# Performance work log

Hardware: AMD Instinct MI355X
Metric: run time of the kernel (lower is better)

The kernel has to match this reference:

```python
import jax, jax.numpy as jnp
import numpy as np

B, L, N_KERNELS = 16, 4096, 512
KSS = [7, 9, 11]


def _make_params():
    """Replicates ROCKET.__init__ random kernel generation (numpy RNG, seed 0).

    Note: the torch code builds Conv1d with padding=2*padding (padding doubled),
    computes the padding from the *float* dilation, and casts dilation to int
    for the conv. We reproduce that exactly.
    """
    rng = np.random.default_rng(0)
    ks_a, d_a, pad_a, w_l, b_l = [], [], [], [], []
    for _ in range(N_KERNELS):
        ks = int(rng.choice(KSS))
        d_f = 2.0 ** rng.uniform(0.0, np.log2((L - 1) // (ks - 1)))
        d = int(d_f)
        p0 = int((ks - 1) * d_f // 2) if rng.integers(2) == 1 else 0
        pad = 2 * p0  # conv1d padding arg is 2*padding in the source
        w = rng.standard_normal(ks).astype(np.float32)
        w -= w.mean()  # weight -= weight.mean() (c_in=1 -> mean over ks)
        b = np.float32(2.0 * (rng.random() - 0.5))
        ks_a.append(ks); d_a.append(d); pad_a.append(pad)
        w_l.append(w); b_l.append(b)
    P = max(pad_a)  # global pad applied once to x; per-kernel offset corrects
    groups = {}
    order = []
    for ks in KSS:
        ids = [i for i in range(N_KERNELS) if ks_a[i] == ks]
        order += ids
        off = np.stack([[P - pad_a[i] + k * d_a[i] for k in range(ks)] for i in ids]).astype(np.int32)
        lout = np.array([L + 2 * pad_a[i] - d_a[i] * (ks - 1) for i in ids], np.int32)
        w = np.stack([w_l[i] for i in ids]).astype(np.float32)
        b = np.array([b_l[i] for i in ids], np.float32)
        groups[ks] = (w, b, off, lout)
    perm = np.argsort(np.array(order)).astype(np.int32)  # grouped -> original order
    return groups, perm, P


def setup_inputs() -> dict:
    key = jax.random.key(0)
    x = jax.random.normal(key, (B, 1, L), dtype=jnp.float32)
    groups, perm, P = _make_params()
    inp = {"x": x, "perm": jnp.asarray(perm), "P": int(P)}
    for gi, ks in enumerate(KSS):
        w, b, off, lout = groups[ks]
        inp[f"w{gi}"] = jnp.asarray(w)
        inp[f"b{gi}"] = jnp.asarray(b)
        inp[f"off{gi}"] = jnp.asarray(off)
        inp[f"lout{gi}"] = jnp.asarray(lout)
    return inp


def _group_feats(x_pad, w, b, off, lout, Lmax, Lp):
    # x_pad: [B, Lp]; w: [G, ks]; off: [G, ks]; lout: [G]
    t = jnp.arange(Lmax)
    out = b[None, :, None]  # [1, G, 1]
    ks = w.shape[-1]
    for k in range(ks):  # ks <= 11 taps of the dilated conv, batched over G kernels
        idx = jnp.clip(off[:, k][:, None] + t[None, :], 0, Lp - 1)  # [G, Lmax]
        out = out + w[:, k][None, :, None] * x_pad[:, idx]  # [B, G, Lmax]
    valid = (t[None, :] < lout[:, None])[None]  # [1, G, Lmax]
    mx = jnp.max(jnp.where(valid, out, jnp.finfo(out.dtype).min), axis=-1)  # [B, G]
    ppv = jnp.where(valid, out > 0, False).sum(-1).astype(out.dtype) / lout[None, :].astype(out.dtype)
    return mx, ppv


def reference(x, w0, b0, off0, lout0, w1, b1, off1, lout1, w2, b2, off2, lout2, perm, P):
    xs = x[:, 0, :]  # c_in = 1
    Lseq = xs.shape[-1]
    Lmax = 2 * Lseq + 16  # static bound: lout <= 2L + max(ks)
    Lp = Lseq + 2 * P
    x_pad = jnp.pad(xs, ((0, 0), (P, P)))
    mxs, ppvs = [], []
    for (w, b, off, lout) in ((w0, b0, off0, lout0), (w1, b1, off1, lout1), (w2, b2, off2, lout2)):
        mx, ppv = _group_feats(x_pad, w, b, off, lout, Lmax, Lp)
        mxs.append(mx)
        ppvs.append(ppv)
    mx = jnp.concatenate(mxs, axis=1)[:, perm]   # [B, n_kernels] original order
    ppv = jnp.concatenate(ppvs, axis=1)[:, perm]
    # torch.cat interleaves (max_i, ppv_i) along feature dim
    return jnp.stack([mx, ppv], axis=2).reshape(x.shape[0], -1)
```

## Files before the change

### kernel.cpp

```cpp
#include <hip/hip_runtime.h>
#include <math.h>

#define LSEQ 4096
#define NK 512
#define NB 16

template <int KS>
__device__ __forceinline__ void rocket_body(
    const float* __restrict__ sx,
    const float* __restrict__ w, const float* __restrict__ bias,
    const int* __restrict__ off, const int* __restrict__ lout,
    int P, int li, int b, int outj,
    float* __restrict__ out, float* smx, int* scnt)
{
    const int tid = threadIdx.x;

    float wk[KS];
#pragma unroll
    for (int k = 0; k < KS; ++k) wk[k] = w[li * KS + k];
    const int o0  = off[li * KS + 0];
    const int o1  = off[li * KS + 1];
    const int d   = o1 - o0;
    const int pad = P - o0;
    const float bi = bias[li];
    const int   Lo = lout[li];

    int t_lo = min(pad, Lo);
    int t_hi = min(Lo, LSEQ - (KS - 1) * d + pad);
    if (t_hi < t_lo) t_hi = t_lo;

    float mx  = -INFINITY;
    int   cnt = 0;

    for (int t = tid; t < t_lo; t += 256) {
        float y = bi;
        int idx = t - pad;
#pragma unroll
        for (int k = 0; k < KS; ++k) {
            int ic = min(max(idx, 0), LSEQ - 1);
            float xv = sx[ic];
            xv = ((unsigned)idx < (unsigned)LSEQ) ? xv : 0.0f;
            y = fmaf(wk[k], xv, y);
            idx += d;
        }
        mx = fmaxf(mx, y); cnt += (y > 0.0f);
    }

    for (int t = t_lo + tid; t < t_hi; t += 256) {
        const float* p = sx + (t - pad);
        float y = bi;
#pragma unroll
        for (int k = 0; k < KS; ++k) y = fmaf(wk[k], p[k * d], y);
        mx = fmaxf(mx, y); cnt += (y > 0.0f);
    }

    for (int t = t_hi + tid; t < Lo; t += 256) {
        float y = bi;
        int idx = t - pad;
#pragma unroll
        for (int k = 0; k < KS; ++k) {
            int ic = min(max(idx, 0), LSEQ - 1);
            float xv = sx[ic];
            xv = ((unsigned)idx < (unsigned)LSEQ) ? xv : 0.0f;
            y = fmaf(wk[k], xv, y);
            idx += d;
        }
        mx = fmaxf(mx, y); cnt += (y > 0.0f);
    }

#pragma unroll
    for (int o = 32; o > 0; o >>= 1) {
        mx = fmaxf(mx, __shfl_down(mx, o, 64));
        cnt += __shfl_down(cnt, o, 64);
    }
    const int wid = tid >> 6;
    if ((tid & 63) == 0) { smx[wid] = mx; scnt[wid] = cnt; }
    __syncthreads();
    if (tid == 0) {
        float m = smx[0]; int c = scnt[0];
#pragma unroll
        for (int i = 1; i < 4; ++i) { m = fmaxf(m, smx[i]); c += scnt[i]; }
        out[b * (2 * NK) + 2 * outj]     = m;
        out[b * (2 * NK) + 2 * outj + 1] = (float)c / (float)Lo;
    }
}

__global__ __launch_bounds__(256) void rocket_lds_kernel(
    const float* __restrict__ x, const int* __restrict__ perm,
    const int* __restrict__ Pp,
    const float* __restrict__ w0, const float* __restrict__ b0,
    const int* __restrict__ off0, const int* __restrict__ l0,
    const float* __restrict__ w1, const float* __restrict__ b1,
    const int* __restrict__ off1, const int* __restrict__ l1,
    const float* __restrict__ w2, const float* __restrict__ b2,
    const int* __restrict__ off2, const int* __restrict__ l2,
    int n0, int n01,
    float* __restrict__ out)
{
    __shared__ float sx[LSEQ];
    __shared__ int   sj;
    __shared__ float smx[4];
    __shared__ int   scnt[4];

    const int gid = blockIdx.x;
    const int b   = blockIdx.y;
    const int tid = threadIdx.x;

    if (perm[tid]       == gid) sj = tid;
    if (perm[tid + 256] == gid) sj = tid + 256;

    const float4* x4 = (const float4*)(x + (size_t)b * LSEQ);
    float4* s4 = (float4*)sx;
#pragma unroll
    for (int i = 0; i < LSEQ / 4 / 256; ++i) s4[tid + 256 * i] = x4[tid + 256 * i];
    __syncthreads();

    const int P = *Pp;
    const int outj = sj;

    if (gid < n0) {
        rocket_body<7>(sx, w0, b0, off0, l0, P, gid, b, outj, out, smx, scnt);
    } else if (gid < n01) {
        rocket_body<9>(sx, w1, b1, off1, l1, P, gid - n0, b, outj, out, smx, scnt);
    } else {
        rocket_body<11>(sx, w2, b2, off2, l2, P, gid - n01, b, outj, out, smx, scnt);
    }
}

extern "C" void kernel_launch(void* const* d_in, const int* in_sizes, int n_in,
                              void* d_out, int out_size, void* d_ws, size_t ws_size,
                              hipStream_t stream) {
    const float* x    = (const float*)d_in[0];
    const int*   perm = (const int*)d_in[1];
    const int*   Pp   = (const int*)d_in[2];
    const float* w0   = (const float*)d_in[3];
    const float* b0   = (const float*)d_in[4];
    const int*   off0 = (const int*)d_in[5];
    const int*   l0   = (const int*)d_in[6];
    const float* w1   = (const float*)d_in[7];
    const float* b1   = (const float*)d_in[8];
    const int*   off1 = (const int*)d_in[9];
    const int*   l1   = (const int*)d_in[10];
    const float* w2   = (const float*)d_in[11];
    const float* b2   = (const float*)d_in[12];
    const int*   off2 = (const int*)d_in[13];
    const int*   l2   = (const int*)d_in[14];

    const int n0 = in_sizes[4];
    const int n1 = in_sizes[8];

    float* out = (float*)d_out;

    rocket_lds_kernel<<<dim3(NK, NB), 256, 0, stream>>>(
        x, perm, Pp, w0, b0, off0, l0, w1, b1, off1, l1, w2, b2, off2, l2,
        n0, n0 + n1, out);
}
```

Measured before the change: 48.95 us.

## Vectorize interior conv with 4 outputs per thread, split taps between LDS copies and global

New measurement: 70.64 us. 44.3% more time.

```diff
diff --git a/kernel.cpp b/kernel.cpp
--- a/kernel.cpp
+++ b/kernel.cpp
@@ -7,7 +7,9 @@
 
 template <int KS>
 __device__ __forceinline__ void rocket_body(
-    const float* __restrict__ sx,
+    const float* __restrict__ sx0,
+    const float* __restrict__ sx1,
+    const float* __restrict__ xg,
     const float* __restrict__ w, const float* __restrict__ bias,
     const int* __restrict__ off, const int* __restrict__ lout,
     int P, int li, int b, int outj,
@@ -28,40 +30,78 @@
     int t_lo = min(pad, Lo);
     int t_hi = min(Lo, LSEQ - (KS - 1) * d + pad);
     if (t_hi < t_lo) t_hi = t_lo;
+    int T0 = (t_lo + 3) & ~3;
+    int T1 = t_hi & ~3;
+    if (T1 < T0) { T0 = 0; T1 = 0; }
 
     float mx  = -INFINITY;
     int   cnt = 0;
 
-    for (int t = tid; t < t_lo; t += 256) {
+    for (int t = tid; t < T0; t += 256) {
         float y = bi;
         int idx = t - pad;
 #pragma unroll
         for (int k = 0; k < KS; ++k) {
-            int ic = min(max(idx, 0), LSEQ - 1);
-            float xv = sx[ic];
-            xv = ((unsigned)idx < (unsigned)LSEQ) ? xv : 0.0f;
+            float xv = ((unsigned)idx < (unsigned)LSEQ) ? xg[idx] : 0.0f;
             y = fmaf(wk[k], xv, y);
             idx += d;
         }
         mx = fmaxf(mx, y); cnt += (y > 0.0f);
     }
 
-    for (int t = t_lo + tid; t < t_hi; t += 256) {
-        const float* p = sx + (t - pad);
-        float y = bi;
-#pragma unroll
-        for (int k = 0; k < KS; ++k) y = fmaf(wk[k], p[k * d], y);
-        mx = fmaxf(mx, y); cnt += (y > 0.0f);
-    }
-
-    for (int t = t_hi + tid; t < Lo; t += 256) {
+    const int nq = (T1 - T0) >> 2;
+    for (int q = tid; q < nq; q += 256) {
+        const int t = T0 + 4 * q;
+        float X[KS][4];
+#pragma unroll
+        for (int k = 0; k < KS; ++k) {
+            const int A = t - pad + k * d;
+            if (k & 1) {
+                const int r = (T0 - pad + k * d) & 3;
+                const float* a = xg + A;
+                if (r == 0) {
+                    const float4 v = *(const float4*)a;
+                    X[k][0] = v.x; X[k][1] = v.y; X[k][2] = v.z; X[k][3] = v.w;
+                } else if (r == 2) {
+                    const float2 v0 = *(const float2*)a;
+                    const float2 v1 = *(const float2*)(a + 2);
+                    X[k][0] = v0.x; X[k][1] = v0.y; X[k][2] = v1.x; X[k][3] = v1.y;
+                } else {
+                    const float2 v = *(const float2*)(a + 1);
+                    X[k][0] = a[0]; X[k][1] = v.x; X[k][2] = v.y; X[k][3] = a[3];
+                }
+            } else {
+                if (((k * d + pad) & 1) == 0) {
+                    const float2 v0 = *(const float2*)(sx0 + A);
+                    const float2 v1 = *(const float2*)(sx0 + A + 2);
+                    X[k][0] = v0.x; X[k][1] = v0.y; X[k][2] = v1.x; X[k][3] = v1.y;
+                } else {
+                    const float2 v0 = *(const float2*)(sx1 + A - 1);
+                    const float2 v1 = *(const float2*)(sx1 + A + 1);
+                    X[k][0] = v0.x; X[k][1] = v0.y; X[k][2] = v1.x; X[k][3] = v1.y;
+                }
+            }
+        }
+        float y0 = bi, y1 = bi, y2 = bi, y3 = bi;
+#pragma unroll
+        for (int k = 0; k < KS; ++k) {
+            y0 = fmaf(wk[k], X[k][0], y0);
+            y1 = fmaf(wk[k], X[k][1], y1);
+            y2 = fmaf(wk[k], X[k][2], y2);
+            y3 = fmaf(wk[k], X[k][3], y3);
+        }
+        mx = fmaxf(mx, y0); cnt += (y0 > 0.0f);
+        mx = fmaxf(mx, y1); cnt += (y1 > 0.0f);
+        mx = fmaxf(mx, y2); cnt += (y2 > 0.0f);
+        mx = fmaxf(mx, y3); cnt += (y3 > 0.0f);
+    }
+
+    for (int t = T1 + tid; t < Lo; t += 256) {
         float y = bi;
         int idx = t - pad;
 #pragma unroll
         for (int k = 0; k < KS; ++k) {
-            int ic = min(max(idx, 0), LSEQ - 1);
-            float xv = sx[ic];
-            xv = ((unsigned)idx < (unsigned)LSEQ) ? xv : 0.0f;
+            float xv = ((unsigned)idx < (unsigned)LSEQ) ? xg[idx] : 0.0f;
             y = fmaf(wk[k], xv, y);
             idx += d;
         }
@@ -85,7 +125,7 @@
     }
 }
 
-__global__ __launch_bounds__(256) void rocket_lds_kernel(
+__global__ __launch_bounds__(256, 4) void rocket_hybrid_kernel(
     const float* __restrict__ x, const int* __restrict__ perm,
     const int* __restrict__ Pp,
     const float* __restrict__ w0, const float* __restrict__ b0,
@@ -97,7 +137,8 @@
     int n0, int n01,
     float* __restrict__ out)
 {
-    __shared__ float sx[LSEQ];
+    __shared__ float sx0[LSEQ];
+    __shared__ float sx1[LSEQ];
     __shared__ int   sj;
     __shared__ float smx[4];
     __shared__ int   scnt[4];
@@ -109,21 +150,30 @@
     if (perm[tid]       == gid) sj = tid;
     if (perm[tid + 256] == gid) sj = tid + 256;
 
-    const float4* x4 = (const float4*)(x + (size_t)b * LSEQ);
-    float4* s4 = (float4*)sx;
-#pragma unroll
-    for (int i = 0; i < LSEQ / 4 / 256; ++i) s4[tid + 256 * i] = x4[tid + 256 * i];
+    const float* xg = x + (size_t)b * LSEQ;
+    const float4* x4 = (const float4*)xg;
+#pragma unroll
+    for (int i = 0; i < LSEQ / 4 / 256; ++i) {
+        const int e4 = tid + 256 * i;
+        const float4 v = x4[e4];
+        const int e = 4 * e4;
+        *(float4*)(sx0 + e) = v;
+        if (e > 0) sx1[e - 1] = v.x;
+        sx1[e]     = v.y;
+        sx1[e + 1] = v.z;
+        sx1[e + 2] = v.w;
+    }
     __syncthreads();
 
     const int P = *Pp;
     const int outj = sj;
 
     if (gid < n0) {
-        rocket_body<7>(sx, w0, b0, off0, l0, P, gid, b, outj, out, smx, scnt);
+        rocket_body<7>(sx0, sx1, xg, w0, b0, off0, l0, P, gid, b, outj, out, smx, scnt);
     } else if (gid < n01) {
-        rocket_body<9>(sx, w1, b1, off1, l1, P, gid - n0, b, outj, out, smx, scnt);
+        rocket_body<9>(sx0, sx1, xg, w1, b1, off1, l1, P, gid - n0, b, outj, out, smx, scnt);
     } else {
-        rocket_body<11>(sx, w2, b2, off2, l2, P, gid - n01, b, outj, out, smx, scnt);
+        rocket_body<11>(sx0, sx1, xg, w2, b2, off2, l2, P, gid - n01, b, outj, out, smx, scnt);
     }
 }
 
@@ -151,7 +201,7 @@
 
     float* out = (float*)d_out;
 
-    rocket_lds_kernel<<<dim3(NK, NB), 256, 0, stream>>>(
+    rocket_hybrid_kernel<<<dim3(NK, NB), 256, 0, stream>>>(
         x, perm, Pp, w0, b0, off0, l0, w1, b1, off1, l1, w2, b2, off2, l2,
         n0, n0 + n1, out);
 }
```

## Process 8 kernels per block and vectorize conv inner loop with shifted LDS copy

Applied to the files above, without the earlier changes.

New measurement: 66.28 us. 35.4% more time.

```diff
diff --git a/kernel.cpp b/kernel.cpp
--- a/kernel.cpp
+++ b/kernel.cpp
@@ -4,6 +4,8 @@
 #define LSEQ 4096
 #define NK 512
 #define NB 16
+#define CK 8
+#define NCH (NK / CK)
 
 template <int KS>
 __device__ __forceinline__ void rocket_body(
@@ -28,11 +30,14 @@
     int t_lo = min(pad, Lo);
     int t_hi = min(Lo, LSEQ - (KS - 1) * d + pad);
     if (t_hi < t_lo) t_hi = t_lo;
+    int T0 = (t_lo + 3) & ~3;
+    int T1 = t_hi & ~3;
+    if (T1 < T0) { T0 = 0; T1 = 0; }
 
     float mx  = -INFINITY;
     int   cnt = 0;
 
-    for (int t = tid; t < t_lo; t += 256) {
+    for (int t = tid; t < T0; t += 256) {
         float y = bi;
         int idx = t - pad;
 #pragma unroll
@@ -46,15 +51,39 @@
         mx = fmaxf(mx, y); cnt += (y > 0.0f);
     }
 
-    for (int t = t_lo + tid; t < t_hi; t += 256) {
-        const float* p = sx + (t - pad);
-        float y = bi;
-#pragma unroll
-        for (int k = 0; k < KS; ++k) y = fmaf(wk[k], p[k * d], y);
-        mx = fmaxf(mx, y); cnt += (y > 0.0f);
-    }
-
-    for (int t = t_hi + tid; t < Lo; t += 256) {
+    int eb[KS];
+#pragma unroll
+    for (int k = 0; k < KS; ++k) {
+        const int A0  = T0 - pad + k * d;
+        const int par = A0 & 1;
+        eb[k] = (-pad + k * d) - par + par * LSEQ;
+    }
+    const int nq = (T1 - T0) >> 2;
+    for (int q = tid; q < nq; q += 256) {
+        const int t = T0 + 4 * q;
+        float X[KS][4];
+#pragma unroll
+        for (int k = 0; k < KS; ++k) {
+            const float* p = sx + (t + eb[k]);
+            const float2 a = *(const float2*)p;
+            const float2 c = *(const float2*)(p + 2);
+            X[k][0] = a.x; X[k][1] = a.y; X[k][2] = c.x; X[k][3] = c.y;
+        }
+        float y0 = bi, y1 = bi, y2 = bi, y3 = bi;
+#pragma unroll
+        for (int k = 0; k < KS; ++k) {
+            y0 = fmaf(wk[k], X[k][0], y0);
+            y1 = fmaf(wk[k], X[k][1], y1);
+            y2 = fmaf(wk[k], X[k][2], y2);
+            y3 = fmaf(wk[k], X[k][3], y3);
+        }
+        mx = fmaxf(mx, y0); cnt += (y0 > 0.0f);
+        mx = fmaxf(mx, y1); cnt += (y1 > 0.0f);
+        mx = fmaxf(mx, y2); cnt += (y2 > 0.0f);
+        mx = fmaxf(mx, y3); cnt += (y3 > 0.0f);
+    }
+
+    for (int t = T1 + tid; t < Lo; t += 256) {
         float y = bi;
         int idx = t - pad;
 #pragma unroll
@@ -85,7 +114,7 @@
     }
 }
 
-__global__ __launch_bounds__(256) void rocket_lds_kernel(
+__global__ __launch_bounds__(256, 4) void rocket_chunk_kernel(
     const float* __restrict__ x, const int* __restrict__ perm,
     const int* __restrict__ Pp,
     const float* __restrict__ w0, const float* __restrict__ b0,
@@ -97,33 +126,53 @@
     int n0, int n01,
     float* __restrict__ out)
 {
-    __shared__ float sx[LSEQ];
-    __shared__ int   sj;
+    __shared__ float sx[2 * LSEQ];
+    __shared__ int   sj[CK];
     __shared__ float smx[4];
     __shared__ int   scnt[4];
 
-    const int gid = blockIdx.x;
-    const int b   = blockIdx.y;
-    const int tid = threadIdx.x;
-
-    if (perm[tid]       == gid) sj = tid;
-    if (perm[tid + 256] == gid) sj = tid + 256;
-
-    const float4* x4 = (const float4*)(x + (size_t)b * LSEQ);
-    float4* s4 = (float4*)sx;
-#pragma unroll
-    for (int i = 0; i < LSEQ / 4 / 256; ++i) s4[tid + 256 * i] = x4[tid + 256 * i];
+    const int chunk = blockIdx.x;
+    const int b     = blockIdx.y;
+    const int tid   = threadIdx.x;
+
+    const int p0 = perm[tid];
+    const int p1 = perm[tid + 256];
+#pragma unroll
+    for (int c = 0; c < CK; ++c) {
+        const int g = chunk + NCH * c;
+        if (p0 == g) sj[c] = tid;
+        if (p1 == g) sj[c] = tid + 256;
+    }
+
+    const float* xg = x + (size_t)b * LSEQ;
+    const float4* x4 = (const float4*)xg;
+#pragma unroll
+    for (int i = 0; i < LSEQ / 4 / 256; ++i) {
+        const int m4 = tid + 256 * i;
+        const int e  = 4 * m4;
+        const float4 v = x4[m4];
+        *(float4*)(sx + e) = v;
+        float nx = __shfl_down(v.x, 1, 64);
+        if ((tid & 63) == 63) nx = (e + 4 < LSEQ) ? xg[e + 4] : 0.0f;
+        float4 u; u.x = v.y; u.y = v.z; u.z = v.w; u.w = nx;
+        *(float4*)(sx + LSEQ + e) = u;
+    }
     __syncthreads();
 
     const int P = *Pp;
-    const int outj = sj;
-
-    if (gid < n0) {
-        rocket_body<7>(sx, w0, b0, off0, l0, P, gid, b, outj, out, smx, scnt);
-    } else if (gid < n01) {
-        rocket_body<9>(sx, w1, b1, off1, l1, P, gid - n0, b, outj, out, smx, scnt);
-    } else {
-        rocket_body<11>(sx, w2, b2, off2, l2, P, gid - n01, b, outj, out, smx, scnt);
+
+#pragma unroll 1
+    for (int c = 0; c < CK; ++c) {
+        const int gid  = chunk + NCH * c;
+        const int outj = sj[c];
+        if (gid < n0) {
+            rocket_body<7>(sx, w0, b0, off0, l0, P, gid, b, outj, out, smx, scnt);
+        } else if (gid < n01) {
+            rocket_body<9>(sx, w1, b1, off1, l1, P, gid - n0, b, outj, out, smx, scnt);
+        } else {
+            rocket_body<11>(sx, w2, b2, off2, l2, P, gid - n01, b, outj, out, smx, scnt);
+        }
+        __syncthreads();
     }
 }
 
@@ -151,7 +200,7 @@
 
     float* out = (float*)d_out;
 
-    rocket_lds_kernel<<<dim3(NK, NB), 256, 0, stream>>>(
+    rocket_chunk_kernel<<<dim3(NCH, NB), 256, 0, stream>>>(
         x, perm, Pp, w0, b0, off0, l0, w1, b1, off1, l1, w2, b2, off2, l2,
         n0, n0 + n1, out);
 }
```
